# Kernel tuning notes

Measured on AMD Instinct MI355X. Metric: run time of the kernel, lower is better.

Reference implementation:

```python
import jax, jax.numpy as jnp
import numpy as np

NUM_EMBEDDINGS = 512
EMBEDDING_DIM = 128
COMMITMENT_COST = 0.6
MID_HR = 100.0
HR_RANGE = 70.0


def setup_inputs() -> dict:
    key = jax.random.key(0)
    k1, k2 = jax.random.split(key)
    inputs = jax.random.normal(k1, (64, 2048, EMBEDDING_DIM), dtype=jnp.float32)
    # torch init: uniform(-1/K, 1/K)
    emb_weight = jax.random.uniform(
        k2, (NUM_EMBEDDINGS, EMBEDDING_DIM), dtype=jnp.float32,
        minval=-1.0 / NUM_EMBEDDINGS, maxval=1.0 / NUM_EMBEDDINGS)
    scaling = jnp.ones((NUM_EMBEDDINGS,), dtype=jnp.float32)
    return {"inputs": inputs, "emb_weight": emb_weight, "scaling": scaling}


def reference(inputs, emb_weight, scaling):
    B, T, D = inputs.shape
    K = emb_weight.shape[0]
    flat = inputs.reshape(-1, D)  # [N, D]
    # squared L2 distances to all codes: [N, K]
    distances = (
        jnp.sum(flat * flat, axis=1, keepdims=True)
        + jnp.sum(emb_weight * emb_weight, axis=1)
        - 2.0 * flat @ emb_weight.T
    )
    hr_values = jnp.linspace(40.0, 180.0, K, dtype=jnp.float32)
    hr_weights = 1.0 + scaling * ((hr_values - MID_HR) / HR_RANGE)  # [K]
    encoding_indices = jnp.argmin(distances * hr_weights[None, :], axis=1)  # [N]
    # one-hot @ codebook == direct gather
    quantized = emb_weight[encoding_indices].reshape(inputs.shape)
    e_latent_loss = jnp.mean((jax.lax.stop_gradient(quantized) - inputs) ** 2)
    q_latent_loss = jnp.mean((quantized - jax.lax.stop_gradient(inputs)) ** 2)
    loss = q_latent_loss + COMMITMENT_COST * e_latent_loss
    # straight-through estimator
    quantized_st = inputs + jax.lax.stop_gradient(quantized - inputs)
    return quantized_st, loss, encoding_indices.reshape(B, T)
```

## Files before the change

### kernel.cpp

```cpp
#include <hip/hip_runtime.h>

#define NCODES 512
#define DIM 128
#define NROWS (64*2048)
#define QN (NROWS*DIM)
#define BLK_ROWS 128
#define NBLOCKS (NROWS/BLK_ROWS)
#define NWAVES 8

typedef __attribute__((ext_vector_type(4))) float f32x4;

#define GLOAD_LDS16(gp, lp) __builtin_amdgcn_global_load_lds( \
    (__attribute__((address_space(1))) void*)(gp), \
    (__attribute__((address_space(3))) void*)(lp), 16, 0, 0)

__global__ void vq_prep(const float* __restrict__ emb, const float* __restrict__ scaling,
                        unsigned char* __restrict__ e8frag,
                        float* __restrict__ wv, float* __restrict__ wse,
                        float* __restrict__ wrcp) {
  int k = blockIdx.x;
  int l = threadIdx.x;
  float2 v = ((const float2*)(emb + k * DIM))[l];
  float ss = v.x * v.x + v.y * v.y;
#pragma unroll
  for (int m = 1; m < 64; m <<= 1) ss += __shfl_xor(ss, m);
  int p = __builtin_amdgcn_cvt_pk_fp8_f32(v.x * 512.0f, v.y * 512.0f, 0, false);
  int t = k >> 4, col = k & 15;
  int c = l >> 4, g = (l >> 2) & 3, jp = l & 3;
  *(unsigned short*)(e8frag + (((t * 4 + c) * 64 + g * 16 + col) << 3) + 2 * jp) =
      (unsigned short)(p & 0xFFFF);
  if (l == 0) {
    float hr = 40.0f + (float)k * (140.0f / 511.0f);
    float wt = 1.0f + scaling[k] * ((hr - 100.0f) * (1.0f / 70.0f));
    wv[k] = wt;
    wse[k] = wt * ss;
    wrcp[k] = 1.0f / wt;
  }
}

struct SmemT {
  unsigned char frag[NCODES * DIM];
  float w[NCODES];
  float wse[NCODES];
  float wrcp[NCODES];
  float lossp[NWAVES];
};

__global__ __launch_bounds__(512, 4) void vq_main(
    const float* __restrict__ x,
    const float* __restrict__ emb32,
    const unsigned char* __restrict__ e8frag,
    const float* __restrict__ wv,
    const float* __restrict__ wse,
    const float* __restrict__ wrcp,
    float* __restrict__ out_q,
    float* __restrict__ out_idx,
    float* __restrict__ out_loss) {
  __shared__ SmemT sm;
  const int tid = threadIdx.x;
  const int wave = tid >> 6, lane = tid & 63;
  const int g = lane >> 4, lr = lane & 15;
  const long rowbase = (long)blockIdx.x * BLK_ROWS + wave * 16;

  float4 xv[4][2];
  {
    const float* xr = x + (rowbase + lr) * DIM + g * 8;
#pragma unroll
    for (int c = 0; c < 4; c++) {
      xv[c][0] = *(const float4*)(xr + c * 32);
      xv[c][1] = *(const float4*)(xr + c * 32 + 4);
    }
  }

  {
#pragma unroll
    for (int i = 0; i < 8; i++) {
      int slot = i * 512 + tid;
      GLOAD_LDS16(e8frag + slot * 16, sm.frag + slot * 16);
    }
    sm.w[tid] = wv[tid]; sm.wse[tid] = wse[tid]; sm.wrcp[tid] = wrcp[tid];
  }

  long a[4];
  float sr[4];
  {
    float ss = 0.f;
#pragma unroll
    for (int c = 0; c < 4; c++) {
      float4 v0 = xv[c][0];
      float4 v1 = xv[c][1];
      ss += v0.x * v0.x + v0.y * v0.y + v0.z * v0.z + v0.w * v0.w;
      ss += v1.x * v1.x + v1.y * v1.y + v1.z * v1.z + v1.w * v1.w;
      int lo = __builtin_amdgcn_cvt_pk_fp8_f32(v0.x, v0.y, 0, false);
      lo = __builtin_amdgcn_cvt_pk_fp8_f32(v0.z, v0.w, lo, true);
      int hi = __builtin_amdgcn_cvt_pk_fp8_f32(v1.x, v1.y, 0, false);
      hi = __builtin_amdgcn_cvt_pk_fp8_f32(v1.z, v1.w, hi, true);
      a[c] = (long)(((unsigned long long)(unsigned)hi << 32) |
                    (unsigned long long)(unsigned)lo);
    }
    ss += __shfl_xor(ss, 16);
    ss += __shfl_xor(ss, 32);
#pragma unroll
    for (int r = 0; r < 4; r++)
      sr[r] = __shfl(ss, g * 4 + r);
  }
  __syncthreads();

  unsigned pmin[4];
#pragma unroll
  for (int r = 0; r < 4; r++) pmin[r] = 0xFFFFFFFFu;

  const long* __restrict__ bbase = (const long*)sm.frag + lane;
#pragma unroll 2
  for (int t = 0; t < 32; t++) {
    const unsigned code = t * 16 + lr;
    const float wt = sm.w[code];
    const float bb = sm.wse[code];
    const float m2w = -2.0f * wt * (1.0f / 512.0f);
    f32x4 acc = {0.f, 0.f, 0.f, 0.f};
#pragma unroll
    for (int c = 0; c < 4; c++) {
      long bf = bbase[(t * 4 + c) * 64];
      acc = __builtin_amdgcn_mfma_f32_16x16x32_fp8_fp8(a[c], bf, acc, 0, 0, 0);
    }
#pragma unroll
    for (int r = 0; r < 4; r++) {
      float v = fmaf(m2w, acc[r], fmaf(wt, sr[r], bb));
      unsigned u = (__builtin_bit_cast(unsigned, v) & 0xFFFFFE00u) | code;
      pmin[r] = min(pmin[r], u);
    }
  }

#pragma unroll
  for (int m = 1; m <= 8; m <<= 1) {
#pragma unroll
    for (int r = 0; r < 4; r++) {
      unsigned o = (unsigned)__shfl_xor((int)pmin[r], m);
      pmin[r] = min(pmin[r], o);
    }
  }

  const uint4* __restrict__ esrc = (const uint4*)emb32;
  uint4* __restrict__ outu = (uint4*)out_q + rowbase * 32;
  const int col = lane & 31;
  const int hi2 = lane >> 5;
  int scode[8];
#pragma unroll
  for (int it = 0; it < 8; it++) {
    const int row0 = 2 * it;
    int c0 = __shfl((int)pmin[row0 & 3], (row0 >> 2) * 16);
    int c1 = __shfl((int)pmin[(row0 + 1) & 3], ((row0 + 1) >> 2) * 16);
    scode[it] = (hi2 ? c1 : c0) & 511;
  }

  uint4 vbuf[8];
#pragma unroll
  for (int j = 0; j < 8; j++)
    vbuf[j] = esrc[scode[j] * 32 + col];

  {
    float l0 = 0.f;
#pragma unroll
    for (int r = 0; r < 4; r++) {
      unsigned wn = pmin[r];
      int ci = (int)(wn & 511u);
      float dist = __builtin_bit_cast(float, wn & 0xFFFFFE00u);
      l0 = fmaf(dist, sm.wrcp[ci], l0);
      if (lr == 0) out_idx[rowbase + g * 4 + r] = (float)ci;
    }
    l0 += __shfl_xor(l0, 16);
    l0 += __shfl_xor(l0, 32);
    if (lane == 0) sm.lossp[wave] = l0;
  }

#pragma unroll
  for (int j = 0; j < 8; j++)
    outu[j * 64 + lane] = vbuf[j];

  __syncthreads();
  if (wave == 0 && lane < NWAVES) {
    float s = sm.lossp[lane];
#pragma unroll
    for (int m = 1; m < NWAVES; m <<= 1) s += __shfl_xor(s, m);
    if (lane == 0) atomicAdd(out_loss, s * (1.6f / (float)QN));
  }
}

extern "C" void kernel_launch(void* const* d_in, const int* in_sizes, int n_in,
                              void* d_out, int out_size, void* d_ws, size_t ws_size,
                              hipStream_t stream) {
  const float* x = (const float*)d_in[0];
  const float* emb = (const float*)d_in[1];
  const float* scaling = (const float*)d_in[2];

  float* out_q = (float*)d_out;
  float* out_loss = out_q + QN;
  float* out_idx = out_q + QN + 1;

  unsigned char* e8frag = (unsigned char*)d_ws;
  float* wv = (float*)((char*)d_ws + NCODES * DIM);
  float* wse = wv + NCODES;
  float* wrcp = wse + NCODES;

  hipMemsetAsync(out_loss, 0, sizeof(float), stream);
  vq_prep<<<NCODES, 64, 0, stream>>>(emb, scaling, e8frag, wv, wse, wrcp);
  vq_main<<<NBLOCKS, 512, 0, stream>>>(x, emb, e8frag, wv, wse, wrcp,
                                       out_q, out_idx, out_loss);
}
```

Baseline: 44.75 us.

## Process two row chunks per wave in 1024-thread blocks to amortize codebook staging

Each block now has 16 waves and covers 512 rows. Every wave handles two 16-row chunks, so the 64KB fp8 codebook is staged into LDS once per 512 rows instead of once per 128. Both chunks' inputs are loaded up front, and the first chunk's gather and stores are interleaved with the second chunk's sweep to overlap memory with MFMA work. In exchange, register pressure rises and launch_bounds(1024,4) may be unachievable given the LDS footprint, so occupancy could drop.

```diff
diff --git a/kernel.cpp b/kernel.cpp
--- a/kernel.cpp
+++ b/kernel.cpp
@@ -4,9 +4,9 @@
 #define DIM 128
 #define NROWS (64*2048)
 #define QN (NROWS*DIM)
-#define BLK_ROWS 128
+#define BLK_ROWS 512
 #define NBLOCKS (NROWS/BLK_ROWS)
-#define NWAVES 8
+#define NWAVES 16
 
 typedef __attribute__((ext_vector_type(4))) float f32x4;
 
@@ -46,7 +46,64 @@
   float lossp[NWAVES];
 };
 
-__global__ __launch_bounds__(512, 4) void vq_main(
+__device__ __forceinline__ void conv_chunk(const float4 xv[4][2], long a[4],
+                                           float sr[4], int g) {
+  float ss = 0.f;
+#pragma unroll
+  for (int c = 0; c < 4; c++) {
+    float4 v0 = xv[c][0];
+    float4 v1 = xv[c][1];
+    ss += v0.x * v0.x + v0.y * v0.y + v0.z * v0.z + v0.w * v0.w;
+    ss += v1.x * v1.x + v1.y * v1.y + v1.z * v1.z + v1.w * v1.w;
+    int lo = __builtin_amdgcn_cvt_pk_fp8_f32(v0.x, v0.y, 0, false);
+    lo = __builtin_amdgcn_cvt_pk_fp8_f32(v0.z, v0.w, lo, true);
+    int hi = __builtin_amdgcn_cvt_pk_fp8_f32(v1.x, v1.y, 0, false);
+    hi = __builtin_amdgcn_cvt_pk_fp8_f32(v1.z, v1.w, hi, true);
+    a[c] = (long)(((unsigned long long)(unsigned)hi << 32) |
+                  (unsigned long long)(unsigned)lo);
+  }
+  ss += __shfl_xor(ss, 16);
+  ss += __shfl_xor(ss, 32);
+#pragma unroll
+  for (int r = 0; r < 4; r++) sr[r] = __shfl(ss, g * 4 + r);
+}
+
+__device__ __forceinline__ void sweep_chunk(const SmemT& sm, int lane, int lr,
+                                            const long a[4], const float sr[4],
+                                            unsigned pmin[4]) {
+#pragma unroll
+  for (int r = 0; r < 4; r++) pmin[r] = 0xFFFFFFFFu;
+  const long* __restrict__ bbase = (const long*)sm.frag + lane;
+#pragma unroll 2
+  for (int t = 0; t < 32; t++) {
+    const unsigned code = t * 16 + lr;
+    const float wt = sm.w[code];
+    const float bb = sm.wse[code];
+    const float m2w = -2.0f * wt * (1.0f / 512.0f);
+    f32x4 acc = {0.f, 0.f, 0.f, 0.f};
+#pragma unroll
+    for (int c = 0; c < 4; c++) {
+      long bf = bbase[(t * 4 + c) * 64];
+      acc = __builtin_amdgcn_mfma_f32_16x16x32_fp8_fp8(a[c], bf, acc, 0, 0, 0);
+    }
+#pragma unroll
+    for (int r = 0; r < 4; r++) {
+      float v = fmaf(m2w, acc[r], fmaf(wt, sr[r], bb));
+      unsigned u = (__builtin_bit_cast(unsigned, v) & 0xFFFFFE00u) | code;
+      pmin[r] = min(pmin[r], u);
+    }
+  }
+#pragma unroll
+  for (int m = 1; m <= 8; m <<= 1) {
+#pragma unroll
+    for (int r = 0; r < 4; r++) {
+      unsigned o = (unsigned)__shfl_xor((int)pmin[r], m);
+      pmin[r] = min(pmin[r], o);
+    }
+  }
+}
+
+__global__ __launch_bounds__(1024, 4) void vq_main(
     const float* __restrict__ x,
     const float* __restrict__ emb32,
     const unsigned char* __restrict__ e8frag,
@@ -60,122 +117,115 @@
   const int tid = threadIdx.x;
   const int wave = tid >> 6, lane = tid & 63;
   const int g = lane >> 4, lr = lane & 15;
-  const long rowbase = (long)blockIdx.x * BLK_ROWS + wave * 16;
-
-  float4 xv[4][2];
-  {
-    const float* xr = x + (rowbase + lr) * DIM + g * 8;
-#pragma unroll
-    for (int c = 0; c < 4; c++) {
-      xv[c][0] = *(const float4*)(xr + c * 32);
-      xv[c][1] = *(const float4*)(xr + c * 32 + 4);
-    }
-  }
-
-  {
-#pragma unroll
-    for (int i = 0; i < 8; i++) {
-      int slot = i * 512 + tid;
-      GLOAD_LDS16(e8frag + slot * 16, sm.frag + slot * 16);
-    }
-    sm.w[tid] = wv[tid]; sm.wse[tid] = wse[tid]; sm.wrcp[tid] = wrcp[tid];
-  }
-
-  long a[4];
-  float sr[4];
-  {
-    float ss = 0.f;
-#pragma unroll
-    for (int c = 0; c < 4; c++) {
-      float4 v0 = xv[c][0];
-      float4 v1 = xv[c][1];
-      ss += v0.x * v0.x + v0.y * v0.y + v0.z * v0.z + v0.w * v0.w;
-      ss += v1.x * v1.x + v1.y * v1.y + v1.z * v1.z + v1.w * v1.w;
-      int lo = __builtin_amdgcn_cvt_pk_fp8_f32(v0.x, v0.y, 0, false);
-      lo = __builtin_amdgcn_cvt_pk_fp8_f32(v0.z, v0.w, lo, true);
-      int hi = __builtin_amdgcn_cvt_pk_fp8_f32(v1.x, v1.y, 0, false);
-      hi = __builtin_amdgcn_cvt_pk_fp8_f32(v1.z, v1.w, hi, true);
-      a[c] = (long)(((unsigned long long)(unsigned)hi << 32) |
-                    (unsigned long long)(unsigned)lo);
-    }
-    ss += __shfl_xor(ss, 16);
-    ss += __shfl_xor(ss, 32);
-#pragma unroll
-    for (int r = 0; r < 4; r++)
-      sr[r] = __shfl(ss, g * 4 + r);
-  }
-  __syncthreads();
-
-  unsigned pmin[4];
-#pragma unroll
-  for (int r = 0; r < 4; r++) pmin[r] = 0xFFFFFFFFu;
-
-  const long* __restrict__ bbase = (const long*)sm.frag + lane;
-#pragma unroll 2
-  for (int t = 0; t < 32; t++) {
-    const unsigned code = t * 16 + lr;
-    const float wt = sm.w[code];
-    const float bb = sm.wse[code];
-    const float m2w = -2.0f * wt * (1.0f / 512.0f);
-    f32x4 acc = {0.f, 0.f, 0.f, 0.f};
-#pragma unroll
-    for (int c = 0; c < 4; c++) {
-      long bf = bbase[(t * 4 + c) * 64];
-      acc = __builtin_amdgcn_mfma_f32_16x16x32_fp8_fp8(a[c], bf, acc, 0, 0, 0);
-    }
-#pragma unroll
-    for (int r = 0; r < 4; r++) {
-      float v = fmaf(m2w, acc[r], fmaf(wt, sr[r], bb));
-      unsigned u = (__builtin_bit_cast(unsigned, v) & 0xFFFFFE00u) | code;
-      pmin[r] = min(pmin[r], u);
-    }
-  }
-
-#pragma unroll
-  for (int m = 1; m <= 8; m <<= 1) {
-#pragma unroll
-    for (int r = 0; r < 4; r++) {
-      unsigned o = (unsigned)__shfl_xor((int)pmin[r], m);
-      pmin[r] = min(pmin[r], o);
-    }
-  }
-
+  const long row0 = (long)blockIdx.x * BLK_ROWS + wave * 16;
+  const long row1 = row0 + 256;
   const uint4* __restrict__ esrc = (const uint4*)emb32;
-  uint4* __restrict__ outu = (uint4*)out_q + rowbase * 32;
   const int col = lane & 31;
   const int hi2 = lane >> 5;
-  int scode[8];
+
+#pragma unroll
+  for (int i = 0; i < 4; i++) {
+    int slot = i * 1024 + tid;
+    GLOAD_LDS16(e8frag + slot * 16, sm.frag + slot * 16);
+  }
+  if (tid < NCODES) {
+    sm.w[tid] = wv[tid]; sm.wse[tid] = wse[tid]; sm.wrcp[tid] = wrcp[tid];
+  }
+  float4 xv0[4][2], xv1[4][2];
+  {
+    const float* xr0 = x + (row0 + lr) * DIM + g * 8;
+    const float* xr1 = x + (row1 + lr) * DIM + g * 8;
+#pragma unroll
+    for (int c = 0; c < 4; c++) {
+      xv0[c][0] = *(const float4*)(xr0 + c * 32);
+      xv0[c][1] = *(const float4*)(xr0 + c * 32 + 4);
+      xv1[c][0] = *(const float4*)(xr1 + c * 32);
+      xv1[c][1] = *(const float4*)(xr1 + c * 32 + 4);
+    }
+  }
+
+  long a0[4]; float sr0[4];
+  conv_chunk(xv0, a0, sr0, g);
+  __syncthreads();
+
+  unsigned pmin0[4];
+  sweep_chunk(sm, lane, lr, a0, sr0, pmin0);
+
+  int scode0[8];
 #pragma unroll
   for (int it = 0; it < 8; it++) {
-    const int row0 = 2 * it;
-    int c0 = __shfl((int)pmin[row0 & 3], (row0 >> 2) * 16);
-    int c1 = __shfl((int)pmin[(row0 + 1) & 3], ((row0 + 1) >> 2) * 16);
-    scode[it] = (hi2 ? c1 : c0) & 511;
-  }
-
-  uint4 vbuf[8];
+    const int r0 = 2 * it;
+    int c0 = __shfl((int)pmin0[r0 & 3], (r0 >> 2) * 16);
+    int c1 = __shfl((int)pmin0[(r0 + 1) & 3], ((r0 + 1) >> 2) * 16);
+    scode0[it] = (hi2 ? c1 : c0) & 511;
+  }
+  uint4 vbuf0[8];
 #pragma unroll
   for (int j = 0; j < 8; j++)
-    vbuf[j] = esrc[scode[j] * 32 + col];
-
+    vbuf0[j] = esrc[scode0[j] * 32 + col];
+
+  float lacc = 0.f;
   {
     float l0 = 0.f;
 #pragma unroll
     for (int r = 0; r < 4; r++) {
-      unsigned wn = pmin[r];
+      unsigned wn = pmin0[r];
       int ci = (int)(wn & 511u);
       float dist = __builtin_bit_cast(float, wn & 0xFFFFFE00u);
       l0 = fmaf(dist, sm.wrcp[ci], l0);
-      if (lr == 0) out_idx[rowbase + g * 4 + r] = (float)ci;
+      if (lr == 0) out_idx[row0 + g * 4 + r] = (float)ci;
     }
     l0 += __shfl_xor(l0, 16);
     l0 += __shfl_xor(l0, 32);
-    if (lane == 0) sm.lossp[wave] = l0;
-  }
-
+    lacc += l0;
+  }
+
+  long a1[4]; float sr1[4];
+  conv_chunk(xv1, a1, sr1, g);
+  unsigned pmin1[4];
+  sweep_chunk(sm, lane, lr, a1, sr1, pmin1);
+
+  {
+    uint4* __restrict__ outu = (uint4*)out_q + row0 * 32;
+#pragma unroll
+    for (int j = 0; j < 8; j++)
+      outu[j * 64 + lane] = vbuf0[j];
+  }
+
+  int scode1[8];
+#pragma unroll
+  for (int it = 0; it < 8; it++) {
+    const int r0 = 2 * it;
+    int c0 = __shfl((int)pmin1[r0 & 3], (r0 >> 2) * 16);
+    int c1 = __shfl((int)pmin1[(r0 + 1) & 3], ((r0 + 1) >> 2) * 16);
+    scode1[it] = (hi2 ? c1 : c0) & 511;
+  }
+  uint4 vbuf1[8];
 #pragma unroll
   for (int j = 0; j < 8; j++)
-    outu[j * 64 + lane] = vbuf[j];
+    vbuf1[j] = esrc[scode1[j] * 32 + col];
+  {
+    float l0 = 0.f;
+#pragma unroll
+    for (int r = 0; r < 4; r++) {
+      unsigned wn = pmin1[r];
+      int ci = (int)(wn & 511u);
+      float dist = __builtin_bit_cast(float, wn & 0xFFFFFE00u);
+      l0 = fmaf(dist, sm.wrcp[ci], l0);
+      if (lr == 0) out_idx[row1 + g * 4 + r] = (float)ci;
+    }
+    l0 += __shfl_xor(l0, 16);
+    l0 += __shfl_xor(l0, 32);
+    lacc += l0;
+  }
+  {
+    uint4* __restrict__ outu = (uint4*)out_q + row1 * 32;
+#pragma unroll
+    for (int j = 0; j < 8; j++)
+      outu[j * 64 + lane] = vbuf1[j];
+  }
+
+  if (lane == 0) sm.lossp[wave] = lacc;
 
   __syncthreads();
   if (wave == 0 && lane < NWAVES) {
@@ -204,6 +254,6 @@
 
   hipMemsetAsync(out_loss, 0, sizeof(float), stream);
   vq_prep<<<NCODES, 64, 0, stream>>>(emb, scaling, e8frag, wv, wse, wrcp);
-  vq_main<<<NBLOCKS, 512, 0, stream>>>(x, emb, e8frag, wv, wse, wrcp,
-                                       out_q, out_idx, out_loss);
-}
+  vq_main<<<NBLOCKS, 1024, 0, stream>>>(x, emb, e8frag, wv, wse, wrcp,
+                                        out_q, out_idx, out_loss);
+}
```

Result: slower. 47.64 us (+6.5%).
